# Optimization experiments

Measured on AMD Instinct MI355X. Metric: run time of the kernel, lower is better.

## Reference

```python
import jax, jax.numpy as jnp
import numpy as np

N_NODES = 100000
N_EDGES = 800000
NODE_DIM = 64
EDGE_DIM = 64
GEO_DIM = 8
GEO_OUT = 32
COND_DIM = 512
N_GRAPHS = 64
JOIN_DIM = EDGE_DIM + GEO_OUT  # 96


def setup_inputs() -> dict:
    key = jax.random.key(0)
    ks = jax.random.split(key, 10)
    return {
        "node_feats": jax.random.normal(ks[0], (N_NODES, NODE_DIM), jnp.float32),
        "edge_index": jax.random.randint(ks[1], (2, N_EDGES), 0, N_NODES, jnp.int64),
        "e_geo": jax.random.normal(ks[2], (N_EDGES, GEO_DIM), jnp.float32),
        "cond": jax.random.normal(ks[3], (N_GRAPHS, COND_DIM), jnp.float32),
        "edge_batch_ids": jax.random.randint(ks[4], (N_EDGES,), 0, N_GRAPHS, jnp.int64),
        "Wn": jax.random.normal(ks[5], (NODE_DIM, EDGE_DIM), jnp.float32) / np.sqrt(NODE_DIM),
        "bn": jnp.zeros((EDGE_DIM,), jnp.float32),
        "Wg": jax.random.normal(ks[6], (GEO_DIM, GEO_OUT), jnp.float32) / np.sqrt(GEO_DIM),
        "bg": jnp.zeros((GEO_OUT,), jnp.float32),
        "Wc": jax.random.normal(ks[7], (COND_DIM, 2 * EDGE_DIM), jnp.float32) / np.sqrt(COND_DIM),
        "bc": jnp.zeros((2 * EDGE_DIM,), jnp.float32),
        "Wx": jax.random.normal(ks[8], (JOIN_DIM, EDGE_DIM), jnp.float32) / np.sqrt(JOIN_DIM),
    }


def reference(node_feats, edge_index, e_geo, cond, edge_batch_ids,
              Wn, bn, Wg, bg, Wc, bc, Wx):
    # n_proj: project node features  [N, node_dim] -> [N, edge_dim]
    n_proj = node_feats @ Wn + bn
    # combine_node_attr 'mul': gather to edge endpoints and multiply  [E, edge_dim]
    src = n_proj[edge_index[0]]
    dst = n_proj[edge_index[1]]
    n_join = src * dst
    # e_geo_linear: [E, geo_dim] -> [E, geo_out]
    eg = e_geo @ Wg + bg
    # join features [E, edge_dim + geo_out]
    join = jnp.concatenate([n_join, eg], axis=-1)
    # FilmFusion: cond_proj -> gamma/beta per graph, gather to edges
    gb = cond @ Wc + bc                      # [B, 2*edge_dim]
    gamma, beta = jnp.split(gb, 2, axis=-1)
    gamma = gamma + 1.0
    gamma_e = gamma[edge_batch_ids]          # [E, edge_dim]
    beta_e = beta[edge_batch_ids]
    # x_linear (bias=False), FiLM modulation, relu
    x = join @ Wx
    return jax.nn.relu(x * gamma_e + beta_e)
```

## Files before the change

kernel.cpp:

```cpp
#include <hip/hip_runtime.h>
#include <hip/hip_bf16.h>

#define N_NODES   100000
#define N_EDGES   800000
#define NODE_DIM  64
#define EDGE_DIM  64
#define GEO_DIM   8
#define GEO_OUT   32
#define COND_DIM  512
#define N_GRAPHS  64

typedef short  bf8   __attribute__((ext_vector_type(8)));
typedef float  f32x4 __attribute__((ext_vector_type(4)));
typedef unsigned short u16x8 __attribute__((ext_vector_type(8)));

__device__ __forceinline__ float b2f(unsigned short u) {
    return __uint_as_float(((unsigned)u) << 16);
}
__device__ __forceinline__ short f2b(float f) {
    unsigned u = __float_as_uint(f);
    u = (u + 0x7FFFu + ((u >> 16) & 1u)) >> 16;
    return (short)u;
}
__device__ __forceinline__ unsigned f2b2(float lo, float hi) {
    __hip_bfloat162 h = __float22bfloat162_rn(make_float2(lo, hi));
    union { __hip_bfloat162 h; unsigned u; } cv;
    cv.h = h;
    return cv.u;
}
__device__ __forceinline__ float rdlane(float v, int l) {
    return __int_as_float(__builtin_amdgcn_readlane(__float_as_int(v), l));
}

__global__ __launch_bounds__(128) void prep_kernel(
        const float* __restrict__ cond, const float* __restrict__ Wc,
        const float* __restrict__ bc,   const float* __restrict__ Wg,
        const float* __restrict__ bg,   const float* __restrict__ Wx,
        float* __restrict__ gamma, float* __restrict__ beta2,
        unsigned short* __restrict__ Bfrag) {
    int t = threadIdx.x;
    int g = blockIdx.x;
    if (g < N_GRAPHS) {
        __shared__ float condl[COND_DIM];
        __shared__ float gbl[128];
        for (int i = t; i < COND_DIM; i += 128) condl[i] = cond[g * COND_DIM + i];
        __syncthreads();
        float acc = bc[t];
        #pragma unroll 8
        for (int k = 0; k < COND_DIM; ++k) acc += condl[k] * Wc[k * 128 + t];
        gbl[t] = acc;
        __syncthreads();
        if (t < 64) {
            float gam = gbl[t] + 1.0f;
            float bet = gbl[64 + t];
            float cv = 0.0f;
            #pragma unroll
            for (int i = 0; i < GEO_OUT; ++i) cv += bg[i] * Wx[(64 + i) * 64 + t];
            gamma[g * 64 + t] = gam;
            beta2[g * 64 + t] = bet + cv * gam;
        }
    } else {
        for (int idx = t; idx < 6144; idx += 128) {
            int j    = idx & 7;
            int lane = (idx >> 3) & 63;
            int ct   = idx >> 9;
            int c    = ct >> 2, tt = ct & 3;
            int k = c * 32 + ((lane >> 4) & 3) * 8 + j;
            int n = tt * 16 + (lane & 15);
            float val;
            if (k < 64) {
                val = Wx[k * 64 + n];
            } else if (k < 72) {
                float s = 0.f;
                #pragma unroll
                for (int i = 0; i < GEO_OUT; ++i)
                    s += Wg[(k - 64) * GEO_OUT + i] * Wx[(64 + i) * 64 + n];
                val = s;
            } else {
                val = 0.f;
            }
            Bfrag[idx] = (unsigned short)f2b(val);
        }
    }
}

__global__ __launch_bounds__(256) void nproj_kernel(
        const float* __restrict__ nf, const float* __restrict__ Wn,
        const float* __restrict__ bn, unsigned short* __restrict__ nprojb) {
    int lane = threadIdx.x & 63;
    int wid    = (blockIdx.x * blockDim.x + threadIdx.x) >> 6;
    int nwaves = (gridDim.x * blockDim.x) >> 6;
    float wcol[64];
    #pragma unroll
    for (int k = 0; k < 64; ++k) wcol[k] = Wn[k * 64 + lane];
    float bnl = bn[lane];
    for (int node = wid; node < N_NODES; node += nwaves) {
        float v = nf[(size_t)node * 64 + lane];
        float a0 = 0.f, a1 = 0.f, a2 = 0.f, a3 = bnl;
        #pragma unroll
        for (int k = 0; k < 64; k += 4) {
            a0 = fmaf(rdlane(v, k    ), wcol[k    ], a0);
            a1 = fmaf(rdlane(v, k + 1), wcol[k + 1], a1);
            a2 = fmaf(rdlane(v, k + 2), wcol[k + 2], a2);
            a3 = fmaf(rdlane(v, k + 3), wcol[k + 3], a3);
        }
        nprojb[(size_t)node * 64 + lane] = (unsigned short)f2b((a0 + a1) + (a2 + a3));
    }
}

__global__ __launch_bounds__(256) void edge_kernel(
        const unsigned short* __restrict__ nprojb,
        const int*   __restrict__ eidx,
        const float* __restrict__ egeo,
        const int*   __restrict__ ebatch,
        const unsigned short* __restrict__ Bfrag,
        const float* __restrict__ gamma,
        const float* __restrict__ beta2,
        float* __restrict__ out) {
    int lane = threadIdx.x & 63;
    int q  = lane >> 4;
    int mm = lane & 15;
    int wv = threadIdx.x >> 6;
    int wid    = (blockIdx.x * blockDim.x + threadIdx.x) >> 6;
    int nwaves = (gridDim.x * blockDim.x) >> 6;

    __shared__ float ldsT[4][16 * 64];
    float* tileb = ldsT[wv];

    bf8 bfrag[3][4];
    #pragma unroll
    for (int c = 0; c < 3; ++c)
        #pragma unroll
        for (int t = 0; t < 4; ++t)
            bfrag[c][t] = *(const bf8*)(Bfrag + (size_t)((c * 4 + t) * 64 + lane) * 8);

    const int NTILES = N_EDGES / 16;
    for (int tile = wid; tile < NTILES; tile += nwaves) {
        int e0 = tile * 16;
        int e  = e0 + mm;
        int s = __builtin_nontemporal_load(eidx + e);
        int d = __builtin_nontemporal_load(eidx + N_EDGES + e);
        int bq[4];
        #pragma unroll
        for (int c = 0; c < 4; ++c)
            bq[c] = __builtin_nontemporal_load(ebatch + e0 + c * 4 + q);

        const u16x8* ps = (const u16x8*)(nprojb + (size_t)s * 64 + q * 8);
        const u16x8* pd = (const u16x8*)(nprojb + (size_t)d * 64 + q * 8);
        u16x8 s0 = ps[0], s1 = ps[4];
        u16x8 d0 = pd[0], d1 = pd[4];

        union { bf8 v; unsigned u[4]; } A0, A1, A2;
        #pragma unroll
        for (int j = 0; j < 8; j += 2) {
            A0.u[j >> 1] = f2b2(b2f(s0[j]) * b2f(d0[j]), b2f(s0[j + 1]) * b2f(d0[j + 1]));
            A1.u[j >> 1] = f2b2(b2f(s1[j]) * b2f(d1[j]), b2f(s1[j + 1]) * b2f(d1[j + 1]));
            A2.u[j >> 1] = 0u;
        }
        if (q == 0) {
            f32x4 g0 = __builtin_nontemporal_load((const f32x4*)(egeo + (size_t)e * 8));
            f32x4 g1 = __builtin_nontemporal_load((const f32x4*)(egeo + (size_t)e * 8 + 4));
            A2.u[0] = f2b2(g0[0], g0[1]);
            A2.u[1] = f2b2(g0[2], g0[3]);
            A2.u[2] = f2b2(g1[0], g1[1]);
            A2.u[3] = f2b2(g1[2], g1[3]);
        }

        f32x4 acc[4];
        #pragma unroll
        for (int t = 0; t < 4; ++t) {
            f32x4 c = {0.f, 0.f, 0.f, 0.f};
            c = __builtin_amdgcn_mfma_f32_16x16x32_bf16(A0.v, bfrag[0][t], c, 0, 0, 0);
            c = __builtin_amdgcn_mfma_f32_16x16x32_bf16(A1.v, bfrag[1][t], c, 0, 0, 0);
            c = __builtin_amdgcn_mfma_f32_16x16x32_bf16(A2.v, bfrag[2][t], c, 0, 0, 0);
            acc[t] = c;
        }

        #pragma unroll
        for (int t = 0; t < 4; ++t)
            #pragma unroll
            for (int i = 0; i < 4; ++i)
                tileb[(q * 4 + i) * 64 + t * 16 + mm] = acc[t][i];
        asm volatile("s_waitcnt lgkmcnt(0)" ::: "memory");

        #pragma unroll
        for (int c = 0; c < 4; ++c) {
            int row = c * 4 + q;
            int b   = bq[c];
            f32x4 v  = *(const f32x4*)&tileb[row * 64 + mm * 4];
            f32x4 gm = *(const f32x4*)(gamma + b * 64 + mm * 4);
            f32x4 bt = *(const f32x4*)(beta2 + b * 64 + mm * 4);
            f32x4 r;
            #pragma unroll
            for (int i = 0; i < 4; ++i) {
                float x = fmaf(v[i], gm[i], bt[i]);
                r[i] = x > 0.f ? x : 0.f;
            }
            __builtin_nontemporal_store(r, (f32x4*)(out + (size_t)e0 * 64 + c * 256 + lane * 4));
        }
    }
}

extern "C" void kernel_launch(void* const* d_in, const int* in_sizes, int n_in,
                              void* d_out, int out_size, void* d_ws, size_t ws_size,
                              hipStream_t stream) {
    const float* node_feats = (const float*)d_in[0];
    const int*   edge_index = (const int*)  d_in[1];
    const float* e_geo      = (const float*)d_in[2];
    const float* cond       = (const float*)d_in[3];
    const int*   ebatch     = (const int*)  d_in[4];
    const float* Wn         = (const float*)d_in[5];
    const float* bn         = (const float*)d_in[6];
    const float* Wg         = (const float*)d_in[7];
    const float* bg         = (const float*)d_in[8];
    const float* Wc         = (const float*)d_in[9];
    const float* bc         = (const float*)d_in[10];
    const float* Wx         = (const float*)d_in[11];
    float* out = (float*)d_out;

    char* ws = (char*)d_ws;
    float*          gamma  = (float*)(ws);
    float*          beta2  = (float*)(ws + 16384);
    unsigned short* Bfrag  = (unsigned short*)(ws + 32768);
    unsigned short* nprojb = (unsigned short*)(ws + 49152);

    hipLaunchKernelGGL(prep_kernel, dim3(65), dim3(128), 0, stream,
                       cond, Wc, bc, Wg, bg, Wx, gamma, beta2, Bfrag);
    hipLaunchKernelGGL(nproj_kernel, dim3(3125), dim3(256), 0, stream,
                       node_feats, Wn, bn, nprojb);
    hipLaunchKernelGGL(edge_kernel, dim3(6250), dim3(256), 0, stream,
                       nprojb, edge_index, e_geo, ebatch, Bfrag, gamma, beta2, out);
}
```

Measured before the change: 372.7 us.

## Switch to fp16 MFMA, software-pipeline edge gathers, stage weights in LDS

```diff
diff --git a/kernel.cpp b/kernel.cpp
--- a/kernel.cpp
+++ b/kernel.cpp
@@ -1,5 +1,4 @@
 #include <hip/hip_runtime.h>
-#include <hip/hip_bf16.h>
 
 #define N_NODES   100000
 #define N_EDGES   800000
@@ -10,26 +9,22 @@
 #define COND_DIM  512
 #define N_GRAPHS  64
 
-typedef short  bf8   __attribute__((ext_vector_type(8)));
-typedef float  f32x4 __attribute__((ext_vector_type(4)));
+typedef float          f32x4 __attribute__((ext_vector_type(4)));
 typedef unsigned short u16x8 __attribute__((ext_vector_type(8)));
-
-__device__ __forceinline__ float b2f(unsigned short u) {
-    return __uint_as_float(((unsigned)u) << 16);
-}
-__device__ __forceinline__ short f2b(float f) {
-    unsigned u = __float_as_uint(f);
-    u = (u + 0x7FFFu + ((u >> 16) & 1u)) >> 16;
-    return (short)u;
-}
-__device__ __forceinline__ unsigned f2b2(float lo, float hi) {
-    __hip_bfloat162 h = __float22bfloat162_rn(make_float2(lo, hi));
-    union { __hip_bfloat162 h; unsigned u; } cv;
+typedef _Float16       f16x8 __attribute__((ext_vector_type(8)));
+typedef _Float16       f16x2 __attribute__((ext_vector_type(2)));
+
+__device__ __forceinline__ unsigned short f2h(float f) {
+    _Float16 h = (_Float16)f;
+    union { _Float16 h; unsigned short u; } cv;
     cv.h = h;
     return cv.u;
 }
-__device__ __forceinline__ float rdlane(float v, int l) {
-    return __int_as_float(__builtin_amdgcn_readlane(__float_as_int(v), l));
+__device__ __forceinline__ f16x2 cvt2h(float lo, float hi) {
+    f16x2 r;
+    r[0] = (_Float16)lo;
+    r[1] = (_Float16)hi;
+    return r;
 }
 
 __global__ __launch_bounds__(128) void prep_kernel(
@@ -79,14 +74,14 @@
             } else {
                 val = 0.f;
             }
-            Bfrag[idx] = (unsigned short)f2b(val);
+            Bfrag[idx] = f2h(val);
         }
     }
 }
 
 __global__ __launch_bounds__(256) void nproj_kernel(
         const float* __restrict__ nf, const float* __restrict__ Wn,
-        const float* __restrict__ bn, unsigned short* __restrict__ nprojb) {
+        const float* __restrict__ bn, unsigned short* __restrict__ nprojh) {
     int lane = threadIdx.x & 63;
     int wid    = (blockIdx.x * blockDim.x + threadIdx.x) >> 6;
     int nwaves = (gridDim.x * blockDim.x) >> 6;
@@ -95,21 +90,22 @@
     for (int k = 0; k < 64; ++k) wcol[k] = Wn[k * 64 + lane];
     float bnl = bn[lane];
     for (int node = wid; node < N_NODES; node += nwaves) {
-        float v = nf[(size_t)node * 64 + lane];
+        int nu = __builtin_amdgcn_readfirstlane(node);
+        const float* row = nf + (size_t)nu * 64;
         float a0 = 0.f, a1 = 0.f, a2 = 0.f, a3 = bnl;
         #pragma unroll
         for (int k = 0; k < 64; k += 4) {
-            a0 = fmaf(rdlane(v, k    ), wcol[k    ], a0);
-            a1 = fmaf(rdlane(v, k + 1), wcol[k + 1], a1);
-            a2 = fmaf(rdlane(v, k + 2), wcol[k + 2], a2);
-            a3 = fmaf(rdlane(v, k + 3), wcol[k + 3], a3);
-        }
-        nprojb[(size_t)node * 64 + lane] = (unsigned short)f2b((a0 + a1) + (a2 + a3));
-    }
-}
-
-__global__ __launch_bounds__(256) void edge_kernel(
-        const unsigned short* __restrict__ nprojb,
+            a0 = fmaf(row[k    ], wcol[k    ], a0);
+            a1 = fmaf(row[k + 1], wcol[k + 1], a1);
+            a2 = fmaf(row[k + 2], wcol[k + 2], a2);
+            a3 = fmaf(row[k + 3], wcol[k + 3], a3);
+        }
+        nprojh[(size_t)nu * 64 + lane] = f2h((a0 + a1) + (a2 + a3));
+    }
+}
+
+__global__ __launch_bounds__(256, 4) void edge_kernel(
+        const unsigned short* __restrict__ nprojh,
         const int*   __restrict__ eidx,
         const float* __restrict__ egeo,
         const int*   __restrict__ ebatch,
@@ -121,58 +117,107 @@
     int q  = lane >> 4;
     int mm = lane & 15;
     int wv = threadIdx.x >> 6;
+
+    __shared__ unsigned short Bl[6144];
+    __shared__ float ldsT[4][16 * 64];
+    float* tileb = ldsT[wv];
+
+    for (int i = threadIdx.x; i < 768; i += 256)
+        ((f32x4*)Bl)[i] = ((const f32x4*)Bfrag)[i];
+    __syncthreads();
+
     int wid    = (blockIdx.x * blockDim.x + threadIdx.x) >> 6;
     int nwaves = (gridDim.x * blockDim.x) >> 6;
-
-    __shared__ float ldsT[4][16 * 64];
-    float* tileb = ldsT[wv];
-
-    bf8 bfrag[3][4];
-    #pragma unroll
-    for (int c = 0; c < 3; ++c)
-        #pragma unroll
-        for (int t = 0; t < 4; ++t)
-            bfrag[c][t] = *(const bf8*)(Bfrag + (size_t)((c * 4 + t) * 64 + lane) * 8);
-
-    const int NTILES = N_EDGES / 16;
-    for (int tile = wid; tile < NTILES; tile += nwaves) {
+    const int NT = N_EDGES / 16;
+
+    int sA, dA, bqA[4];
+    int bqC[4];
+    u16x8 s0, s1, d0, d1;
+    f32x4 g0 = {0,0,0,0}, g1 = {0,0,0,0};
+
+    int tile = wid;
+    {
         int e0 = tile * 16;
-        int e  = e0 + mm;
-        int s = __builtin_nontemporal_load(eidx + e);
-        int d = __builtin_nontemporal_load(eidx + N_EDGES + e);
-        int bq[4];
+        sA = __builtin_nontemporal_load(eidx + e0 + mm);
+        dA = __builtin_nontemporal_load(eidx + N_EDGES + e0 + mm);
         #pragma unroll
         for (int c = 0; c < 4; ++c)
-            bq[c] = __builtin_nontemporal_load(ebatch + e0 + c * 4 + q);
-
-        const u16x8* ps = (const u16x8*)(nprojb + (size_t)s * 64 + q * 8);
-        const u16x8* pd = (const u16x8*)(nprojb + (size_t)d * 64 + q * 8);
-        u16x8 s0 = ps[0], s1 = ps[4];
-        u16x8 d0 = pd[0], d1 = pd[4];
-
-        union { bf8 v; unsigned u[4]; } A0, A1, A2;
-        #pragma unroll
-        for (int j = 0; j < 8; j += 2) {
-            A0.u[j >> 1] = f2b2(b2f(s0[j]) * b2f(d0[j]), b2f(s0[j + 1]) * b2f(d0[j + 1]));
-            A1.u[j >> 1] = f2b2(b2f(s1[j]) * b2f(d1[j]), b2f(s1[j + 1]) * b2f(d1[j + 1]));
-            A2.u[j >> 1] = 0u;
-        }
+            bqA[c] = __builtin_nontemporal_load(ebatch + e0 + c * 4 + q);
+        const u16x8* ps = (const u16x8*)(nprojh + (size_t)sA * 64 + q * 8);
+        const u16x8* pd = (const u16x8*)(nprojh + (size_t)dA * 64 + q * 8);
+        s0 = ps[0]; s1 = ps[4];
+        d0 = pd[0]; d1 = pd[4];
         if (q == 0) {
-            f32x4 g0 = __builtin_nontemporal_load((const f32x4*)(egeo + (size_t)e * 8));
-            f32x4 g1 = __builtin_nontemporal_load((const f32x4*)(egeo + (size_t)e * 8 + 4));
-            A2.u[0] = f2b2(g0[0], g0[1]);
-            A2.u[1] = f2b2(g0[2], g0[3]);
-            A2.u[2] = f2b2(g1[0], g1[1]);
-            A2.u[3] = f2b2(g1[2], g1[3]);
+            g0 = __builtin_nontemporal_load((const f32x4*)(egeo + (size_t)(e0 + mm) * 8));
+            g1 = __builtin_nontemporal_load((const f32x4*)(egeo + (size_t)(e0 + mm) * 8 + 4));
+        }
+        #pragma unroll
+        for (int c = 0; c < 4; ++c) bqC[c] = bqA[c];
+        int tn = tile + nwaves;
+        if (tn < NT) {
+            int e0n = tn * 16;
+            sA = __builtin_nontemporal_load(eidx + e0n + mm);
+            dA = __builtin_nontemporal_load(eidx + N_EDGES + e0n + mm);
+            #pragma unroll
+            for (int c = 0; c < 4; ++c)
+                bqA[c] = __builtin_nontemporal_load(ebatch + e0n + c * 4 + q);
+        }
+    }
+
+    for (; tile < NT; tile += nwaves) {
+        int e0  = tile * 16;
+        int tn  = tile + nwaves;
+        int tnn = tn + nwaves;
+        bool hasN  = tn  < NT;
+        bool hasNN = tnn < NT;
+
+        union HU { u16x8 v; f16x2 h[4]; unsigned u[4]; f16x8 f; };
+        HU S0, S1, D0, D1, A0, A1, A2;
+        S0.v = s0; S1.v = s1; D0.v = d0; D1.v = d1;
+        #pragma unroll
+        for (int j = 0; j < 4; ++j) {
+            A0.h[j] = S0.h[j] * D0.h[j];
+            A1.h[j] = S1.h[j] * D1.h[j];
+            A2.u[j] = 0u;
+        }
+        if (q == 0) {
+            A2.h[0] = cvt2h(g0[0], g0[1]);
+            A2.h[1] = cvt2h(g0[2], g0[3]);
+            A2.h[2] = cvt2h(g1[0], g1[1]);
+            A2.h[3] = cvt2h(g1[2], g1[3]);
+        }
+
+        int sB, dB, bqB[4];
+        if (hasNN) {
+            int e0nn = tnn * 16;
+            sB = __builtin_nontemporal_load(eidx + e0nn + mm);
+            dB = __builtin_nontemporal_load(eidx + N_EDGES + e0nn + mm);
+            #pragma unroll
+            for (int c = 0; c < 4; ++c)
+                bqB[c] = __builtin_nontemporal_load(ebatch + e0nn + c * 4 + q);
+        }
+        if (hasN) {
+            const u16x8* ps = (const u16x8*)(nprojh + (size_t)sA * 64 + q * 8);
+            const u16x8* pd = (const u16x8*)(nprojh + (size_t)dA * 64 + q * 8);
+            s0 = ps[0]; s1 = ps[4];
+            d0 = pd[0]; d1 = pd[4];
+            int e0n = tn * 16;
+            if (q == 0) {
+                g0 = __builtin_nontemporal_load((const f32x4*)(egeo + (size_t)(e0n + mm) * 8));
+                g1 = __builtin_nontemporal_load((const f32x4*)(egeo + (size_t)(e0n + mm) * 8 + 4));
+            }
         }
 
         f32x4 acc[4];
         #pragma unroll
         for (int t = 0; t < 4; ++t) {
             f32x4 c = {0.f, 0.f, 0.f, 0.f};
-            c = __builtin_amdgcn_mfma_f32_16x16x32_bf16(A0.v, bfrag[0][t], c, 0, 0, 0);
-            c = __builtin_amdgcn_mfma_f32_16x16x32_bf16(A1.v, bfrag[1][t], c, 0, 0, 0);
-            c = __builtin_amdgcn_mfma_f32_16x16x32_bf16(A2.v, bfrag[2][t], c, 0, 0, 0);
+            c = __builtin_amdgcn_mfma_f32_16x16x32_f16(
+                    A0.f, *(const f16x8*)(Bl + (size_t)((0 * 4 + t) * 64 + lane) * 8), c, 0, 0, 0);
+            c = __builtin_amdgcn_mfma_f32_16x16x32_f16(
+                    A1.f, *(const f16x8*)(Bl + (size_t)((1 * 4 + t) * 64 + lane) * 8), c, 0, 0, 0);
+            c = __builtin_amdgcn_mfma_f32_16x16x32_f16(
+                    A2.f, *(const f16x8*)(Bl + (size_t)((2 * 4 + t) * 64 + lane) * 8), c, 0, 0, 0);
             acc[t] = c;
         }
 
@@ -182,11 +227,10 @@
             for (int i = 0; i < 4; ++i)
                 tileb[(q * 4 + i) * 64 + t * 16 + mm] = acc[t][i];
         asm volatile("s_waitcnt lgkmcnt(0)" ::: "memory");
-
         #pragma unroll
         for (int c = 0; c < 4; ++c) {
             int row = c * 4 + q;
-            int b   = bq[c];
+            int b   = bqC[c];
             f32x4 v  = *(const f32x4*)&tileb[row * 64 + mm * 4];
             f32x4 gm = *(const f32x4*)(gamma + b * 64 + mm * 4);
             f32x4 bt = *(const f32x4*)(beta2 + b * 64 + mm * 4);
@@ -197,6 +241,14 @@
                 r[i] = x > 0.f ? x : 0.f;
             }
             __builtin_nontemporal_store(r, (f32x4*)(out + (size_t)e0 * 64 + c * 256 + lane * 4));
+        }
+
+        #pragma unroll
+        for (int c = 0; c < 4; ++c) bqC[c] = bqA[c];
+        if (hasNN) {
+            sA = sB; dA = dB;
+            #pragma unroll
+            for (int c = 0; c < 4; ++c) bqA[c] = bqB[c];
         }
     }
 }
@@ -222,12 +274,12 @@
     float*          gamma  = (float*)(ws);
     float*          beta2  = (float*)(ws + 16384);
     unsigned short* Bfrag  = (unsigned short*)(ws + 32768);
-    unsigned short* nprojb = (unsigned short*)(ws + 49152);
+    unsigned short* nprojh = (unsigned short*)(ws + 49152);
 
     hipLaunchKernelGGL(prep_kernel, dim3(65), dim3(128), 0, stream,
                        cond, Wc, bc, Wg, bg, Wx, gamma, beta2, Bfrag);
     hipLaunchKernelGGL(nproj_kernel, dim3(3125), dim3(256), 0, stream,
-                       node_feats, Wn, bn, nprojb);
-    hipLaunchKernelGGL(edge_kernel, dim3(6250), dim3(256), 0, stream,
-                       nprojb, edge_index, e_geo, ebatch, Bfrag, gamma, beta2, out);
-}
+                       node_feats, Wn, bn, nprojh);
+    hipLaunchKernelGGL(edge_kernel, dim3(3125), dim3(256), 0, stream,
+                       nprojh, edge_index, e_geo, ebatch, Bfrag, gamma, beta2, out);
+}
```

Result: no change. 369.8 us (-0.8%).
